# Performance work log

Measured on AMD Instinct MI355X. Metric: run time of the kernel, lower is better.

## Reference

```python
import jax, jax.numpy as jnp
import numpy as np
from jax import lax

B = 512          # scoring batch size
NC = 10          # n_classes
N_LAB = 256      # int(B * plb), plb = 0.5 (labeled indices are the first N_LAB)
TOL = 1e-3       # gtg_t
MAX_ITER = 30    # gtg_i
INTERM = 128
CH = [64, 128, 256, 512]
SZ = [32, 16, 8, 4]
EMB = 512


def setup_inputs() -> dict:
    key = jax.random.key(0)
    ks = jax.random.split(key, 16)
    inp = {}
    for i, (c, s) in enumerate(zip(CH, SZ)):
        inp["feat%d" % i] = jax.random.normal(ks[i], (B, c, s, s), jnp.float32)
        inp["conv_w%d" % i] = jax.random.normal(ks[4 + i], (c, c, 3, 3), jnp.float32) * 0.05
        inp["conv_b%d" % i] = jnp.zeros((c,), jnp.float32)
        inp["bn_g%d" % i] = jnp.ones((c,), jnp.float32)
        inp["bn_b%d" % i] = jnp.zeros((c,), jnp.float32)
        inp["lin_w%d" % i] = jax.random.normal(ks[8 + i], (INTERM, c), jnp.float32) * 0.05
        inp["lin_b%d" % i] = jnp.zeros((INTERM,), jnp.float32)
    inp["fin_w"] = jax.random.normal(ks[12], (1, 4 * INTERM), jnp.float32) * 0.05
    inp["fin_b"] = jnp.zeros((1,), jnp.float32)
    inp["embedds"] = jax.random.normal(ks[13], (B, EMB), jnp.float32)
    inp["labels"] = jax.random.randint(ks[14], (B,), 0, NC)
    return inp


def _branch(x, cw, cb, g, b, lw, lb):
    # Conv3x3(same) -> BatchNorm (train mode, batch stats, eps=1e-5) -> ReLU -> GAP -> Linear -> ReLU
    y = lax.conv_general_dilated(x, cw, (1, 1), 'SAME',
                                 dimension_numbers=('NCHW', 'OIHW', 'NCHW')) + cb[None, :, None, None]
    m = y.mean(axis=(0, 2, 3), keepdims=True)
    v = ((y - m) ** 2).mean(axis=(0, 2, 3), keepdims=True)  # biased variance (train-mode BN)
    y = jax.nn.relu(g[None, :, None, None] * (y - m) * lax.rsqrt(v + 1e-5) + b[None, :, None, None])
    y = y.mean(axis=(2, 3))  # AvgPool2d(feature_size) == global average pool -> [B, C]
    return jax.nn.relu(y @ lw.T + lb)


def _gtg(E, labels):
    # get_A_e_d: pairwise euclidean distances clamped to [0.1, 1.0]
    sq = jnp.sum(E * E, axis=1)
    d2 = jnp.maximum(sq[:, None] + sq[None, :] - 2.0 * (E @ E.T), 0.0)
    A0 = jnp.clip(jnp.sqrt(d2), 0.1, 1.0)
    # rbf kernel: 7th nearest neighbor (ascending for 'e_d') gives per-sample sigma
    seventh = E[jnp.argsort(A0, axis=1)[:, 6]]
    sig = jnp.clip(jnp.sqrt(jnp.sum((E - seventh) ** 2, axis=1)), 0.1, 1.0)
    A = jnp.clip(jnp.exp(-(A0 ** 2) / (sig[:, None] * sig[None, :])), 0.0, 1.0)
    # threshold strategy 'mean' with AM_function == 'e_d': A = where(A > mean(A), 1, A)
    A = jnp.where(A > A.mean(), 1.0, A)
    # AM_strategy 'mixed' with 'e_d': flip only the labeled x labeled block
    A = A.at[:N_LAB, :N_LAB].set(1.0 - A[:N_LAB, :N_LAB])
    # get_X: one-hot for labeled (first N_LAB), uniform 1/NC for unlabeled
    X0 = jnp.concatenate([jax.nn.one_hot(labels[:N_LAB], NC, dtype=jnp.float32),
                          jnp.full((B - N_LAB, NC), 1.0 / NC, jnp.float32)], axis=0)
    hist0 = jnp.zeros((B, MAX_ITER), jnp.float32)

    def cond(c):
        return (c[3] > TOL) & (c[2] < MAX_ITER)

    def body(c):
        X, h, i, _ = c
        Xn = X * (A @ X)
        Xn = Xn / jnp.sum(Xn, axis=1, keepdims=True)
        ent = -jnp.sum(jnp.where(Xn > 0, Xn * jnp.log(Xn), 0.0), axis=1)
        h = lax.dynamic_update_slice(h, ent[:, None], (0, i))
        return (Xn, h, i + 1, jnp.linalg.norm(Xn - X))

    X, h, _, _ = lax.while_loop(cond, body, (X0, hist0, jnp.int32(0), jnp.float32(jnp.inf)))
    return h.mean(axis=1), X  # ent_strategy == 'mean'


def reference(feat0, feat1, feat2, feat3,
              conv_w0, conv_b0, bn_g0, bn_b0, lin_w0, lin_b0,
              conv_w1, conv_b1, bn_g1, bn_b1, lin_w1, lin_b1,
              conv_w2, conv_b2, bn_g2, bn_b2, lin_w2, lin_b2,
              conv_w3, conv_b3, bn_g3, bn_b3, lin_w3, lin_b3,
              fin_w, fin_b, embedds, labels):
    o0 = _branch(feat0, conv_w0, conv_b0, bn_g0, bn_b0, lin_w0, lin_b0)
    o1 = _branch(feat1, conv_w1, conv_b1, bn_g1, bn_b1, lin_w1, lin_b1)
    o2 = _branch(feat2, conv_w2, conv_b2, bn_g2, bn_b2, lin_w2, lin_b2)
    o3 = _branch(feat3, conv_w3, conv_b3, bn_g3, bn_b3, lin_w3, lin_b3)
    y_pred = (jnp.concatenate([o0, o1, o2, o3], axis=1) @ fin_w.T + fin_b)[:, 0]
    y_true, X = _gtg(embedds, labels)
    labeled_mask = jnp.arange(B) < N_LAB
    return (y_pred, y_true, X, labeled_mask)
```

## Files before the change

### kernel.cpp

```cpp
#include <hip/hip_runtime.h>
#include <hip/hip_bf16.h>
#include <math.h>

static constexpr int kNC = 10;
static constexpr int kNLab = 256;
static constexpr int kMaxIter = 30;

using short8 = __attribute__((ext_vector_type(8))) short;
using f32x4  = __attribute__((ext_vector_type(4))) float;

__device__ __forceinline__ unsigned short f2bf(float f) {
  unsigned int u = __float_as_uint(f);
  u += 0x7FFFu + ((u >> 16) & 1u);
  return (unsigned short)(u >> 16);
}
__device__ __forceinline__ float bf2f(unsigned short u) {
  return __uint_as_float(((unsigned int)u) << 16);
}

template <int C, int S>
__global__ __launch_bounds__(256) void xpack_kernel(const float* __restrict__ x,
                                                    unsigned short* __restrict__ xp) {
  __shared__ float t[C][S + 1];
  const int n = blockIdx.x / S, h = blockIdx.x % S;
  const float* src = x + (size_t)n * C * S * S;
  for (int e = threadIdx.x; e < C * S; e += 256) {
    int c = e / S, w = e % S;
    t[c][w] = src[((size_t)c * S + h) * S + w];
  }
  __syncthreads();
  unsigned short* dst = xp + ((size_t)(n * S + h) * S) * C;
  for (int e = threadIdx.x; e < C * S; e += 256) {
    int w = e / C, c = e % C;
    dst[(size_t)w * C + c] = f2bf(t[c][w]);
  }
}

__global__ void wpack_all(const float* __restrict__ w0, const float* __restrict__ w1,
                          const float* __restrict__ w2, const float* __restrict__ w3,
                          unsigned short* __restrict__ wpk) {
  int idx = blockIdx.x * 256 + threadIdx.x;
  if (idx >= 3133440) return;
  const float* w; int C, off;
  if (idx < 36864)        { w = w0; C = 64;  off = 0; }
  else if (idx < 184320)  { w = w1; C = 128; off = 36864; }
  else if (idx < 774144)  { w = w2; C = 256; off = 184320; }
  else                    { w = w3; C = 512; off = 774144; }
  int e = idx - off;
  int CO16T = C / 16, CIK = C / 32;
  int e8 = e & 7, l = (e >> 3) & 63;
  int rest = e >> 9;
  int co16 = rest % CO16T;
  int rest2 = rest / CO16T;
  int cik = rest2 % CIK, tap = rest2 / CIK;
  int co = co16 * 16 + (l & 15);
  int ci = cik * 32 + (l >> 4) * 8 + e8;
  wpk[idx] = f2bf(w[((size_t)co * C + ci) * 9 + tap]);
}

template <int C, int S, int NI, int NR, int WV, int BF, int MODE>
__global__ __launch_bounds__(WV * 64)
void conv_mfma(const unsigned short* __restrict__ xp, const unsigned short* __restrict__ wpk,
               const float* __restrict__ bias, unsigned short* __restrict__ y,
               float* __restrict__ psum, float* __restrict__ psq, int npart, int partBase,
               const float* __restrict__ scale, const float* __restrict__ shift,
               float* __restrict__ pp, int pxGlobalBase) {
  constexpr int SS = S * S;
  constexpr int PXB = NI * NR * S;
  constexpr int TPB = WV * 64;
  constexpr int HR = NR + 2, HC = S + 2;
  constexpr int CIK = C / 32, CO16T = C / 16;
  constexpr int UNITS = NI * HR * HC * 4;
  constexpr int NU = (UNITS + TPB - 1) / TPB;
  static_assert(WV * BF * 16 == PXB, "wave px mismatch");
  static_assert(MODE != 2 || BF == 4, "MODE2 assumes 64px/wave");
  __shared__ __align__(16) char xs[NI * HR * HC * 80];

  const int tid = threadIdx.x;
  const int wv = tid >> 6, l = tid & 63, l15 = l & 15, l4 = l >> 4;
  const int coblk = blockIdx.y;
  const int co_base = coblk * 64;
  const int pxb = blockIdx.x * PXB;
  const int n_t = pxb / SS;
  const int r0 = (pxb % SS) / S;

  int pxoff[BF];
#pragma unroll
  for (int bf = 0; bf < BF; ++bf) {
    int pxloc = wv * (BF * 16) + bf * 16 + l15;
    int ii = pxloc / (NR * S);
    int rr = (pxloc % (NR * S)) / S;
    int cc = pxloc % S;
    pxoff[bf] = ((ii * HR + rr) * HC + cc) * 80 + l4 * 16;
  }

  f32x4 acc[4][BF];
#pragma unroll
  for (int a = 0; a < 4; ++a)
#pragma unroll
    for (int b = 0; b < BF; ++b) acc[a][b] = (f32x4){0.f, 0.f, 0.f, 0.f};

  uint4 vreg[NU];
  auto loadU = [&](int cik) {
#pragma unroll
    for (int k = 0; k < NU; ++k) {
      int u = tid + k * TPB;
      uint4 v = {0u, 0u, 0u, 0u};
      if (u < UNITS) {
        int k16 = u & 3;
        int t = u >> 2;
        int hc = t % HC;
        int t2 = t / HC;
        int hr = t2 % HR;
        int ii = t2 / HR;
        int row = r0 + hr - 1, col = hc - 1;
        if (row >= 0 && row < S && col >= 0 && col < S)
          v = *(const uint4*)(xp + ((size_t)((n_t + ii) * S + row) * S + col) * C + cik * 32 + k16 * 8);
      }
      vreg[k] = v;
    }
  };

  loadU(0);
  for (int cik = 0; cik < CIK; ++cik) {
    __syncthreads();
#pragma unroll
    for (int k = 0; k < NU; ++k) {
      int u = tid + k * TPB;
      if (u < UNITS) *(uint4*)(xs + (u >> 2) * 80 + (u & 3) * 16) = vreg[k];
    }
    __syncthreads();
    if (cik + 1 < CIK) loadU(cik + 1);
#pragma unroll
    for (int tap = 0; tap < 9; ++tap) {
      const int tapoff = ((tap / 3) * HC + (tap % 3)) * 80;
      short8 wf[4], xf[BF];
#pragma unroll
      for (int af = 0; af < 4; ++af)
        wf[af] = *(const short8*)(wpk + ((size_t)((tap * CIK + cik) * CO16T + coblk * 4 + af) * 64 + l) * 8);
#pragma unroll
      for (int bf = 0; bf < BF; ++bf)
        xf[bf] = *(const short8*)(xs + pxoff[bf] + tapoff);
#pragma unroll
      for (int af = 0; af < 4; ++af)
#pragma unroll
        for (int bf = 0; bf < BF; ++bf)
          acc[af][bf] = __builtin_amdgcn_mfma_f32_16x16x32_bf16(wf[af], xf[bf], acc[af][bf], 0, 0, 0);
    }
  }

#pragma unroll
  for (int af = 0; af < 4; ++af) {
    const int co0 = co_base + af * 16 + l4 * 4;
    float4 bv = *(const float4*)(bias + co0);
    float s[4] = {0.f, 0.f, 0.f, 0.f}, q[4] = {0.f, 0.f, 0.f, 0.f};
    float4 sc4, sh4;
    if (MODE == 2) {
      sc4 = *(const float4*)(scale + co0);
      sh4 = *(const float4*)(shift + co0);
    }
#pragma unroll
    for (int bf = 0; bf < BF; ++bf) {
      float o[4];
#pragma unroll
      for (int r = 0; r < 4; ++r) o[r] = acc[af][bf][r] + ((const float*)&bv)[r];
      if (MODE == 0) {
        ushort4 pk;
        pk.x = f2bf(o[0]); pk.y = f2bf(o[1]); pk.z = f2bf(o[2]); pk.w = f2bf(o[3]);
        size_t px = (size_t)(pxb + wv * (BF * 16) + bf * 16 + l15);
        *(ushort4*)(y + px * C + co0) = pk;
      }
      if (MODE == 2) {
#pragma unroll
        for (int r = 0; r < 4; ++r)
          s[r] += fmaxf(fmaf(((const float*)&sc4)[r], o[r], ((const float*)&sh4)[r]), 0.f);
      } else {
#pragma unroll
        for (int r = 0; r < 4; ++r) { s[r] += o[r]; q[r] += o[r] * o[r]; }
      }
    }
#pragma unroll
    for (int m = 1; m < 16; m <<= 1) {
#pragma unroll
      for (int r = 0; r < 4; ++r) {
        s[r] += __shfl_xor(s[r], m);
        if (MODE != 2) q[r] += __shfl_xor(q[r], m);
      }
    }
    if (l15 == 0) {
      if (MODE == 2) {
        int n = (pxGlobalBase + pxb) / SS;
        int qw = ((pxGlobalBase + pxb) % SS) / 64 + wv;
#pragma unroll
        for (int r = 0; r < 4; ++r)
          pp[((size_t)(n * C + co0 + r)) * 16 + qw] = s[r];
      } else {
        int part = partBase + blockIdx.x * WV + wv;
#pragma unroll
        for (int r = 0; r < 4; ++r) {
          psum[(size_t)(co0 + r) * npart + part] = s[r];
          psq[(size_t)(co0 + r) * npart + part] = q[r];
        }
      }
    }
  }
}

__global__ __launch_bounds__(256)
void stats2_kernel(const float* __restrict__ psum, const float* __restrict__ psq,
                   const float* __restrict__ g, const float* __restrict__ bb,
                   float* __restrict__ scale, float* __restrict__ shift,
                   int npart, float invN) {
  int c = blockIdx.x;
  __shared__ float rs[256], rq[256];
  float s = 0.f, q = 0.f;
  for (int p = threadIdx.x; p < npart; p += 256) {
    s += psum[(size_t)c * npart + p];
    q += psq[(size_t)c * npart + p];
  }
  rs[threadIdx.x] = s; rq[threadIdx.x] = q;
  __syncthreads();
  for (int st = 128; st; st >>= 1) {
    if (threadIdx.x < st) { rs[threadIdx.x] += rs[threadIdx.x + st]; rq[threadIdx.x] += rq[threadIdx.x + st]; }
    __syncthreads();
  }
  if (threadIdx.x == 0) {
    float m = rs[0] * invN;
    float v = rq[0] * invN - m * m;
    float sc = g[c] / sqrtf(v + 1e-5f);
    scale[c] = sc;
    shift[c] = bb[c] - m * sc;
  }
}

template <int C, int S>
__global__ __launch_bounds__(256)
void pool_lin(const unsigned short* __restrict__ y, const float* __restrict__ scale,
              const float* __restrict__ shift, const float* __restrict__ lw,
              const float* __restrict__ lb, float* __restrict__ oc, int brOff) {
  constexpr int SS = S * S;
  int n = blockIdx.x;
  const unsigned short* yr = y + (size_t)n * SS * C;
  __shared__ float pl[C];
  if (C >= 256) {
    for (int co = threadIdx.x; co < C; co += 256) {
      float sc = scale[co], sh = shift[co], s = 0.f;
      for (int p = 0; p < SS; ++p) s += fmaxf(fmaf(sc, bf2f(yr[(size_t)p * C + co]), sh), 0.f);
      pl[co] = s * (1.f / SS);
    }
  } else {
    constexpr int G = 256 / C;
    int co = threadIdx.x % C;
    int sl = threadIdx.x / C;
    float sc = scale[co], sh = shift[co], s = 0.f;
    for (int p = sl; p < SS; p += G) s += fmaxf(fmaf(sc, bf2f(yr[(size_t)p * C + co]), sh), 0.f);
    __shared__ float red[256];
    red[threadIdx.x] = s;
    __syncthreads();
    if (threadIdx.x < C) {
      float t = 0.f;
      for (int gg = 0; gg < G; ++gg) t += red[gg * C + co];
      pl[co] = t * (1.f / SS);
    }
  }
  __syncthreads();
  if (threadIdx.x < 128) {
    int j = threadIdx.x;
    const float* wr = lw + (size_t)j * C;
    float s = 0.f;
    for (int t = 0; t < C; ++t) s = fmaf(pl[t], wr[t], s);
    s += lb[j];
    oc[n * 512 + brOff + j] = fmaxf(s, 0.f);
  }
}

__global__ void poolfin_kernel(const float* __restrict__ pp, float* __restrict__ pooled) {
  int i = blockIdx.x * 256 + threadIdx.x;
  if (i >= 512 * 64) return;
  float s = 0.f;
  for (int qn = 0; qn < 16; ++qn) s += pp[(size_t)i * 16 + qn];
  pooled[i] = s * (1.f / 1024.f);
}

__global__ void lin_kernel(const float* __restrict__ pooled, const float* __restrict__ lw,
                           const float* __restrict__ lb, float* __restrict__ oc,
                           int C, int brOff) {
  int idx = blockIdx.x * 256 + threadIdx.x;
  if (idx >= 512 * 128) return;
  int j = idx & 127, n = idx >> 7;
  const float4* pr = (const float4*)(pooled + (size_t)n * C);
  const float4* wr = (const float4*)(lw + (size_t)j * C);
  float s = 0.f;
  for (int t = 0; t < C / 4; ++t) {
    float4 a = pr[t], b = wr[t];
    s += a.x * b.x + a.y * b.y + a.z * b.z + a.w * b.w;
  }
  s += lb[j];
  oc[n * 512 + brOff + j] = fmaxf(s, 0.f);
}

__global__ void ypred_kernel(const float* __restrict__ oc, const float* __restrict__ fw,
                             const float* __restrict__ fb, float* __restrict__ out) {
  int wv = threadIdx.x >> 6, l = threadIdx.x & 63;
  int n = blockIdx.x * 4 + wv;
  float s = 0.f;
  for (int k = l; k < 512; k += 64) s += oc[n * 512 + k] * fw[k];
#pragma unroll
  for (int m = 32; m; m >>= 1) s += __shfl_down(s, m);
  if (l == 0) out[n] = s + fb[0];
}

__global__ void sqnorm_kernel(const float* __restrict__ E, float* __restrict__ sq) {
  int wv = threadIdx.x >> 6, l = threadIdx.x & 63;
  int n = blockIdx.x * 4 + wv;
  const float* row = E + (size_t)n * 512;
  float s = 0.f;
  for (int k = l; k < 512; k += 64) { float v = row[k]; s += v * v; }
#pragma unroll
  for (int m = 32; m; m >>= 1) s += __shfl_down(s, m);
  if (l == 0) sq[n] = s;
}

__global__ __launch_bounds__(256) void a0_kernel(const float* __restrict__ E,
                                                 const float* __restrict__ sq,
                                                 float* __restrict__ A0) {
  int bi = blockIdx.x / 32, bj = blockIdx.x % 32;
  int ti = threadIdx.x % 16, tj = threadIdx.x / 16;
  __shared__ float Ei[16][68], Ej[16][68];
  float acc = 0.f;
  for (int k0 = 0; k0 < 512; k0 += 64) {
    for (int e = threadIdx.x; e < 1024; e += 256) {
      int rr = e >> 6, cc = e & 63;
      Ei[rr][cc] = E[(size_t)(bi * 16 + rr) * 512 + k0 + cc];
      Ej[rr][cc] = E[(size_t)(bj * 16 + rr) * 512 + k0 + cc];
    }
    __syncthreads();
#pragma unroll 16
    for (int kk = 0; kk < 64; ++kk) acc = fmaf(Ei[tj][kk], Ej[ti][kk], acc);
    __syncthreads();
  }
  int i = bi * 16 + tj, j = bj * 16 + ti;
  float d2 = fmaxf(sq[i] + sq[j] - 2.f * acc, 0.f);
  A0[(size_t)i * 512 + j] = fminf(fmaxf(sqrtf(d2), 0.1f), 1.0f);
}

__global__ void seventh_kernel(const float* __restrict__ A0, int* __restrict__ idx7) {
  int i = blockIdx.x * 256 + threadIdx.x;
  if (i >= 512) return;
  float v[7]; int ix[7];
#pragma unroll
  for (int t = 0; t < 7; ++t) { v[t] = 3.4e38f; ix[t] = 0; }
  const float* row = A0 + (size_t)i * 512;
  for (int j = 0; j < 512; ++j) {
    float a = row[j];
    if (a < v[6]) {
      int pos = 6;
      while (pos > 0 && a < v[pos - 1]) { v[pos] = v[pos - 1]; ix[pos] = ix[pos - 1]; --pos; }
      v[pos] = a; ix[pos] = j;
    }
  }
  idx7[i] = ix[6];
}

__global__ void sig_kernel(const float* __restrict__ E, const int* __restrict__ idx7,
                           float* __restrict__ sig) {
  int wv = threadIdx.x >> 6, l = threadIdx.x & 63;
  int n = blockIdx.x * 4 + wv;
  const float* r1 = E + (size_t)n * 512;
  const float* r2 = E + (size_t)idx7[n] * 512;
  float s = 0.f;
  for (int k = l; k < 512; k += 64) { float d = r1[k] - r2[k]; s += d * d; }
#pragma unroll
  for (int m = 32; m; m >>= 1) s += __shfl_down(s, m);
  if (l == 0) sig[n] = fminf(fmaxf(sqrtf(s), 0.1f), 1.0f);
}

__global__ void aexp_kernel(const float* __restrict__ A0, const float* __restrict__ sig,
                            float* __restrict__ A, float* __restrict__ part) {
  int t = blockIdx.x * 256 + threadIdx.x;
  int base = t * 4;
  int i = base >> 9, j0 = base & 511;
  float si = sig[i];
  float4 a = *(const float4*)(A0 + base);
  float4 o;
  o.x = fminf(fmaxf(expf(-a.x * a.x / (si * sig[j0 + 0])), 0.f), 1.f);
  o.y = fminf(fmaxf(expf(-a.y * a.y / (si * sig[j0 + 1])), 0.f), 1.f);
  o.z = fminf(fmaxf(expf(-a.z * a.z / (si * sig[j0 + 2])), 0.f), 1.f);
  o.w = fminf(fmaxf(expf(-a.w * a.w / (si * sig[j0 + 3])), 0.f), 1.f);
  *(float4*)(A + base) = o;
  float lsum = o.x + o.y + o.z + o.w;
#pragma unroll
  for (int m = 32; m; m >>= 1) lsum += __shfl_down(lsum, m);
  __shared__ float sred[4];
  if ((threadIdx.x & 63) == 0) sred[threadIdx.x >> 6] = lsum;
  __syncthreads();
  if (threadIdx.x == 0) part[blockIdx.x] = sred[0] + sred[1] + sred[2] + sred[3];
}

__global__ void meanred_kernel(const float* __restrict__ part, float* __restrict__ meanA) {
  if (threadIdx.x == 0 && blockIdx.x == 0) {
    float s = 0.f;
    for (int p = 0; p < 256; ++p) s += part[p];
    meanA[0] = s * (1.0f / 262144.0f);
  }
}

__global__ void thresh_kernel(float* __restrict__ A, const float* __restrict__ meanA) {
  int t = blockIdx.x * 256 + threadIdx.x;
  int base = t * 4;
  int i = base >> 9, j0 = base & 511;
  float m = meanA[0];
  float4 v = *(const float4*)(A + base);
  v.x = v.x > m ? 1.f : v.x;
  v.y = v.y > m ? 1.f : v.y;
  v.z = v.z > m ? 1.f : v.z;
  v.w = v.w > m ? 1.f : v.w;
  if (i < kNLab && j0 < kNLab) {
    v.x = 1.f - v.x; v.y = 1.f - v.y; v.z = 1.f - v.z; v.w = 1.f - v.w;
  }
  *(float4*)(A + base) = v;
}

__global__ __launch_bounds__(256)
void gtg_iters16(const float* __restrict__ A, const int* __restrict__ labels,
                 float* __restrict__ Xg, float* __restrict__ diffPart,
                 float* __restrict__ out, int* __restrict__ flags) {
  constexpr int NB = 16, RPB = 32;
  const int b = blockIdx.x, tid = threadIdx.x;
  const int pg = tid & 31, rg = tid >> 5;
  __shared__ float Xs[512][kNC];
  __shared__ float dred[8];

  float a[4][16];
  {
    const int gr0 = b * RPB + rg * 4;
#pragma unroll
    for (int rr = 0; rr < 4; ++rr) {
      const float* Ar = A + (size_t)(gr0 + rr) * 512 + pg;
#pragma unroll
      for (int jj = 0; jj < 16; ++jj) a[rr][jj] = Ar[32 * jj];
    }
  }
  for (int e = tid; e < 512 * kNC; e += 256) {
    int r = e / kNC, c = e % kNC;
    Xs[r][c] = (r < kNLab) ? ((labels[r] == c) ? 1.f : 0.f) : 0.1f;
  }
  __syncthreads();

  float entsum[4] = {0.f, 0.f, 0.f, 0.f};
  int ph = 0;
  for (int it = 0; it < kMaxIter; ++it) {
    if (it > 0) {
      float s = 0.f;
      for (int q = 0; q < NB; ++q) s += diffPart[(it - 1) * NB + q];
      if (sqrtf(s) <= 0.001f) break;
    }
    float ax[4][kNC];
#pragma unroll
    for (int rr = 0; rr < 4; ++rr)
#pragma unroll
      for (int c = 0; c < kNC; ++c) ax[rr][c] = 0.f;
#pragma unroll
    for (int jj = 0; jj < 16; ++jj) {
      int j = pg + 32 * jj;
      float xv[kNC];
#pragma unroll
      for (int c = 0; c < kNC; ++c) xv[c] = Xs[j][c];
#pragma unroll
      for (int rr = 0; rr < 4; ++rr) {
        float av = a[rr][jj];
#pragma unroll
        for (int c = 0; c < kNC; ++c) ax[rr][c] = fmaf(av, xv[c], ax[rr][c]);
      }
    }
#pragma unroll
    for (int m = 1; m < 32; m <<= 1)
#pragma unroll
      for (int rr = 0; rr < 4; ++rr)
#pragma unroll
        for (int c = 0; c < kNC; ++c) ax[rr][c] += __shfl_xor(ax[rr][c], m);
    if (pg == 0) {
      const int gr0 = b * RPB + rg * 4;
      float dpsum = 0.f;
#pragma unroll
      for (int rr = 0; rr < 4; ++rr) {
        int gi = gr0 + rr;
        float xn[kNC], ssum = 0.f;
#pragma unroll
        for (int c = 0; c < kNC; ++c) { xn[c] = Xs[gi][c] * ax[rr][c]; ssum += xn[c]; }
        float ent = 0.f;
#pragma unroll
        for (int c = 0; c < kNC; ++c) {
          float xv = xn[c] / ssum;
          if (xv > 0.f) ent -= xv * logf(xv);
          float d = xv - Xs[gi][c];
          dpsum += d * d;
          Xg[gi * kNC + c] = xv;
        }
        entsum[rr] += ent;
      }
      dred[rg] = dpsum;
    }
    __syncthreads();
    if (tid == 0) {
      float s2 = 0.f;
#pragma unroll
      for (int q = 0; q < 8; ++q) s2 += dred[q];
      diffPart[it * NB + b] = s2;
    }
    __syncthreads();
    __threadfence();
    if (tid == 0)
      __hip_atomic_store(&flags[b], ph + 1, __ATOMIC_RELEASE, __HIP_MEMORY_SCOPE_AGENT);
    if (tid < NB) {
      while (__hip_atomic_load(&flags[tid], __ATOMIC_ACQUIRE, __HIP_MEMORY_SCOPE_AGENT) <= ph)
        __builtin_amdgcn_s_sleep(1);
    }
    ++ph;
    __syncthreads();
    for (int e = tid; e < 512 * kNC; e += 256) Xs[e / kNC][e % kNC] = Xg[e];
    __syncthreads();
  }

  if (pg == 0) {
    const int gr0 = b * RPB + rg * 4;
#pragma unroll
    for (int rr = 0; rr < 4; ++rr) {
      int gi = gr0 + rr;
      out[512 + gi] = entsum[rr] * (1.0f / 30.0f);
      out[6144 + gi] = (gi < kNLab) ? 1.0f : 0.0f;
    }
  }
  for (int e = tid; e < RPB * kNC; e += 256) {
    int gi = b * RPB + e / kNC;
    out[1024 + gi * kNC + e % kNC] = Xs[gi][e % kNC];
  }
}

extern "C" void kernel_launch(void* const* d_in, const int* in_sizes, int n_in,
                              void* d_out, int out_size, void* d_ws, size_t ws_size,
                              hipStream_t stream) {
  (void)in_sizes; (void)n_in; (void)out_size;

  const float* feat[4]; const float* cw[4]; const float* cbp[4];
  const float* bg[4]; const float* bbp[4]; const float* lw[4]; const float* lbp[4];
  for (int b = 0; b < 4; ++b) {
    int base = b * 7;
    feat[b] = (const float*)d_in[base + 0];
    cw[b]  = (const float*)d_in[base + 1];
    cbp[b] = (const float*)d_in[base + 2];
    bg[b]  = (const float*)d_in[base + 3];
    bbp[b] = (const float*)d_in[base + 4];
    lw[b]  = (const float*)d_in[base + 5];
    lbp[b] = (const float*)d_in[base + 6];
  }
  const float* finw = (const float*)d_in[28];
  const float* finb = (const float*)d_in[29];
  const float* emb  = (const float*)d_in[30];
  const int* labels = (const int*)d_in[31];
  float* out = (float*)d_out;

  float* wsf = (float*)d_ws;
  unsigned short* xpad = (unsigned short*)wsf;
  unsigned short* yP   = (unsigned short*)(wsf + 4194304);
  unsigned short* wpk  = (unsigned short*)(wsf + 12582912);
  size_t off = 14149632;
  float* psum = wsf + off; off += 524288;
  float* psq  = wsf + off; off += 524288;
  float* pp   = wsf + off; off += 524288;
  float* scale = wsf + off; off += 512;
  float* shift = wsf + off; off += 512;
  float* pooled = wsf + off; off += 491520;
  float* oc = wsf + off; off += 262144;
  float* sq = wsf + off; off += 512;
  float* A0 = wsf + off; off += 262144;
  float* Am = wsf + off; off += 262144;
  float* sig = wsf + off; off += 512;
  int* idx7 = (int*)(wsf + off); off += 512;
  float* meanPart = wsf + off; off += 256;
  float* meanA = wsf + off; off += 4;
  float* Xg = wsf + off; off += 5120;
  float* diffPart = wsf + off; off += 512;
  int* flags = (int*)(wsf + off); off += 32;
  size_t yb0_off = off;
  unsigned short* yB0 = (unsigned short*)(wsf + yb0_off);
  const bool bigB0 = ws_size >= (yb0_off + 16777216) * sizeof(float);

  unsigned short* wpkB[4] = {wpk, wpk + 36864, wpk + 184320, wpk + 774144};

  wpack_all<<<(3133440 + 255) / 256, 256, 0, stream>>>(cw[0], cw[1], cw[2], cw[3], wpk);

  for (int c = 0; c < 2; ++c) {
    xpack_kernel<128, 16><<<256 * 16, 256, 0, stream>>>(feat[1] + (size_t)c * 8388608, xpad);
    conv_mfma<128, 16, 1, 8, 4, 2, 0><<<dim3(512, 2), 256, 0, stream>>>(
        xpad, wpkB[1], cbp[1], yP + (size_t)c * 8388608, psum, psq, 4096, c * 2048,
        nullptr, nullptr, nullptr, 0);
  }
  stats2_kernel<<<128, 256, 0, stream>>>(psum, psq, bg[1], bbp[1], scale, shift, 4096, 1.f / 131072.f);
  pool_lin<128, 16><<<512, 256, 0, stream>>>(yP, scale, shift, lw[1], lbp[1], oc, 128);

  xpack_kernel<256, 8><<<512 * 8, 256, 0, stream>>>(feat[2], xpad);
  conv_mfma<256, 8, 2, 8, 4, 2, 0><<<dim3(256, 4), 256, 0, stream>>>(
      xpad, wpkB[2], cbp[2], yP, psum, psq, 1024, 0, nullptr, nullptr, nullptr, 0);
  stats2_kernel<<<256, 256, 0, stream>>>(psum, psq, bg[2], bbp[2], scale, shift, 1024, 1.f / 32768.f);
  pool_lin<256, 8><<<512, 256, 0, stream>>>(yP, scale, shift, lw[2], lbp[2], oc, 256);

  xpack_kernel<512, 4><<<512 * 4, 256, 0, stream>>>(feat[3], xpad);
  conv_mfma<512, 4, 8, 4, 4, 2, 0><<<dim3(64, 8), 256, 0, stream>>>(
      xpad, wpkB[3], cbp[3], yP, psum, psq, 256, 0, nullptr, nullptr, nullptr, 0);
  stats2_kernel<<<512, 256, 0, stream>>>(psum, psq, bg[3], bbp[3], scale, shift, 256, 1.f / 8192.f);
  pool_lin<512, 4><<<512, 256, 0, stream>>>(yP, scale, shift, lw[3], lbp[3], oc, 384);

  if (bigB0) {
    for (int c = 0; c < 4; ++c) {
      xpack_kernel<64, 32><<<128 * 32, 256, 0, stream>>>(feat[0] + (size_t)c * 8388608, xpad);
      conv_mfma<64, 32, 1, 8, 4, 4, 0><<<dim3(512, 1), 256, 0, stream>>>(
          xpad, wpkB[0], cbp[0], yB0 + (size_t)c * 8388608, psum, psq, 8192, c * 2048,
          nullptr, nullptr, nullptr, 0);
    }
    stats2_kernel<<<64, 256, 0, stream>>>(psum, psq, bg[0], bbp[0], scale, shift, 8192, 1.f / 524288.f);
    pool_lin<64, 32><<<512, 256, 0, stream>>>(yB0, scale, shift, lw[0], lbp[0], oc, 0);
  } else {
    for (int c = 0; c < 4; ++c) {
      xpack_kernel<64, 32><<<128 * 32, 256, 0, stream>>>(feat[0] + (size_t)c * 8388608, xpad);
      conv_mfma<64, 32, 1, 8, 4, 4, 1><<<dim3(512, 1), 256, 0, stream>>>(
          xpad, wpkB[0], cbp[0], nullptr, psum, psq, 8192, c * 2048, nullptr, nullptr, nullptr, 0);
    }
    stats2_kernel<<<64, 256, 0, stream>>>(psum, psq, bg[0], bbp[0], scale, shift, 8192, 1.f / 524288.f);
    for (int c = 0; c < 4; ++c) {
      xpack_kernel<64, 32><<<128 * 32, 256, 0, stream>>>(feat[0] + (size_t)c * 8388608, xpad);
      conv_mfma<64, 32, 1, 8, 4, 4, 2><<<dim3(512, 1), 256, 0, stream>>>(
          xpad, wpkB[0], cbp[0], nullptr, nullptr, nullptr, 0, 0, scale, shift, pp, c * 131072);
    }
    poolfin_kernel<<<128, 256, 0, stream>>>(pp, pooled);
    lin_kernel<<<256, 256, 0, stream>>>(pooled, lw[0], lbp[0], oc, 64, 0);
  }

  ypred_kernel<<<128, 256, 0, stream>>>(oc, finw, finb, out);
  sqnorm_kernel<<<128, 256, 0, stream>>>(emb, sq);
  a0_kernel<<<1024, 256, 0, stream>>>(emb, sq, A0);
  seventh_kernel<<<2, 256, 0, stream>>>(A0, idx7);
  sig_kernel<<<128, 256, 0, stream>>>(emb, idx7, sig);
  aexp_kernel<<<256, 256, 0, stream>>>(A0, sig, Am, meanPart);
  meanred_kernel<<<1, 64, 0, stream>>>(meanPart, meanA);
  thresh_kernel<<<256, 256, 0, stream>>>(Am, meanA);

  hipMemsetAsync(flags, 0, 64, stream);
  gtg_iters16<<<16, 256, 0, stream>>>(Am, labels, Xg, diffPart, out, flags);
}
```

Before: 1.003 ms.

## Run GTG iterations in one block and skip fixed labeled rows

Replaces the 16-block GTG iteration kernel, which synchronised through global flags and atomics on every iteration, with a single 1024-thread block that uses only __syncthreads. It relies on the labeled rows staying one-hot: their contribution A[unlabeled, labeled]·onehot is computed once up front, and only the 256 unlabeled rows are updated each iteration. Labeled outputs (zero entropy, one-hot X) are written directly. This removes the cross-block barrier latency and half the matvec work, at the cost of using only one CU and assuming a labeled row's class sum is never zero.

```diff
diff --git a/kernel.cpp b/kernel.cpp
--- a/kernel.cpp
+++ b/kernel.cpp
@@ -421,119 +421,138 @@
   *(float4*)(A + base) = v;
 }
 
-__global__ __launch_bounds__(256)
-void gtg_iters16(const float* __restrict__ A, const int* __restrict__ labels,
-                 float* __restrict__ Xg, float* __restrict__ diffPart,
-                 float* __restrict__ out, int* __restrict__ flags) {
-  constexpr int NB = 16, RPB = 32;
-  const int b = blockIdx.x, tid = threadIdx.x;
-  const int pg = tid & 31, rg = tid >> 5;
-  __shared__ float Xs[512][kNC];
-  __shared__ float dred[8];
-
-  float a[4][16];
+__global__ __launch_bounds__(1024)
+void gtg1(const float* __restrict__ A, const int* __restrict__ labels,
+          float* __restrict__ out) {
+  const int tid = threadIdx.x;
+  const int w = tid >> 6, l = tid & 63;
+  const int rc = w & 3, g = w >> 2;
+  const int i = rc * 64 + l;
+  __shared__ float Xs[256][12];
+  __shared__ float Ls[256][12];
+  __shared__ float axred[4][256][12];
+  __shared__ float dredw[4];
+  __shared__ int labs[256];
+
+  if (tid < 256) labs[tid] = labels[tid];
+  for (int e = tid; e < 256 * 12; e += 1024)
+    (&Xs[0][0])[e] = ((e % 12) < 10) ? 0.1f : 0.f;
+  __syncthreads();
+
+  const float* Ar = A + (size_t)(256 + i) * 512;
+  float areg[64];
+#pragma unroll
+  for (int q = 0; q < 16; ++q) {
+    float4 v = *(const float4*)(Ar + 256 + g * 64 + q * 4);
+    areg[q * 4 + 0] = v.x; areg[q * 4 + 1] = v.y;
+    areg[q * 4 + 2] = v.z; areg[q * 4 + 3] = v.w;
+  }
   {
-    const int gr0 = b * RPB + rg * 4;
-#pragma unroll
-    for (int rr = 0; rr < 4; ++rr) {
-      const float* Ar = A + (size_t)(gr0 + rr) * 512 + pg;
-#pragma unroll
-      for (int jj = 0; jj < 16; ++jj) a[rr][jj] = Ar[32 * jj];
-    }
-  }
-  for (int e = tid; e < 512 * kNC; e += 256) {
-    int r = e / kNC, c = e % kNC;
-    Xs[r][c] = (r < kNLab) ? ((labels[r] == c) ? 1.f : 0.f) : 0.1f;
+    float lp[10];
+#pragma unroll
+    for (int c = 0; c < 10; ++c) lp[c] = 0.f;
+    for (int q = 0; q < 16; ++q) {
+      float4 v = *(const float4*)(Ar + g * 64 + q * 4);
+      float av[4] = {v.x, v.y, v.z, v.w};
+#pragma unroll
+      for (int k = 0; k < 4; ++k) {
+        int lab = labs[g * 64 + q * 4 + k];
+#pragma unroll
+        for (int c = 0; c < 10; ++c) lp[c] += (lab == c) ? av[k] : 0.f;
+      }
+    }
+    *(float4*)&axred[g][i][0] = make_float4(lp[0], lp[1], lp[2], lp[3]);
+    *(float4*)&axred[g][i][4] = make_float4(lp[4], lp[5], lp[6], lp[7]);
+    *(float2*)&axred[g][i][8] = make_float2(lp[8], lp[9]);
   }
   __syncthreads();
-
-  float entsum[4] = {0.f, 0.f, 0.f, 0.f};
-  int ph = 0;
+  if (g == 0) {
+    float s[10];
+#pragma unroll
+    for (int c = 0; c < 10; ++c) s[c] = 0.f;
+#pragma unroll
+    for (int q = 0; q < 4; ++q) {
+      float4 a0 = *(const float4*)&axred[q][i][0];
+      float4 a1 = *(const float4*)&axred[q][i][4];
+      float2 a2 = *(const float2*)&axred[q][i][8];
+      s[0] += a0.x; s[1] += a0.y; s[2] += a0.z; s[3] += a0.w;
+      s[4] += a1.x; s[5] += a1.y; s[6] += a1.z; s[7] += a1.w;
+      s[8] += a2.x; s[9] += a2.y;
+    }
+    *(float4*)&Ls[i][0] = make_float4(s[0], s[1], s[2], s[3]);
+    *(float4*)&Ls[i][4] = make_float4(s[4], s[5], s[6], s[7]);
+    *(float2*)&Ls[i][8] = make_float2(s[8], s[9]);
+  }
+  __syncthreads();
+
+  float entsum = 0.f;
+  float nrm2 = 1e30f;
   for (int it = 0; it < kMaxIter; ++it) {
-    if (it > 0) {
-      float s = 0.f;
-      for (int q = 0; q < NB; ++q) s += diffPart[(it - 1) * NB + q];
-      if (sqrtf(s) <= 0.001f) break;
-    }
-    float ax[4][kNC];
-#pragma unroll
-    for (int rr = 0; rr < 4; ++rr)
-#pragma unroll
-      for (int c = 0; c < kNC; ++c) ax[rr][c] = 0.f;
-#pragma unroll
-    for (int jj = 0; jj < 16; ++jj) {
-      int j = pg + 32 * jj;
-      float xv[kNC];
-#pragma unroll
-      for (int c = 0; c < kNC; ++c) xv[c] = Xs[j][c];
-#pragma unroll
-      for (int rr = 0; rr < 4; ++rr) {
-        float av = a[rr][jj];
-#pragma unroll
-        for (int c = 0; c < kNC; ++c) ax[rr][c] = fmaf(av, xv[c], ax[rr][c]);
-      }
-    }
-#pragma unroll
-    for (int m = 1; m < 32; m <<= 1)
-#pragma unroll
-      for (int rr = 0; rr < 4; ++rr)
-#pragma unroll
-        for (int c = 0; c < kNC; ++c) ax[rr][c] += __shfl_xor(ax[rr][c], m);
-    if (pg == 0) {
-      const int gr0 = b * RPB + rg * 4;
-      float dpsum = 0.f;
-#pragma unroll
-      for (int rr = 0; rr < 4; ++rr) {
-        int gi = gr0 + rr;
-        float xn[kNC], ssum = 0.f;
-#pragma unroll
-        for (int c = 0; c < kNC; ++c) { xn[c] = Xs[gi][c] * ax[rr][c]; ssum += xn[c]; }
-        float ent = 0.f;
-#pragma unroll
-        for (int c = 0; c < kNC; ++c) {
-          float xv = xn[c] / ssum;
-          if (xv > 0.f) ent -= xv * logf(xv);
-          float d = xv - Xs[gi][c];
-          dpsum += d * d;
-          Xg[gi * kNC + c] = xv;
-        }
-        entsum[rr] += ent;
-      }
-      dred[rg] = dpsum;
-    }
-    __syncthreads();
-    if (tid == 0) {
-      float s2 = 0.f;
-#pragma unroll
-      for (int q = 0; q < 8; ++q) s2 += dred[q];
-      diffPart[it * NB + b] = s2;
-    }
-    __syncthreads();
-    __threadfence();
-    if (tid == 0)
-      __hip_atomic_store(&flags[b], ph + 1, __ATOMIC_RELEASE, __HIP_MEMORY_SCOPE_AGENT);
-    if (tid < NB) {
-      while (__hip_atomic_load(&flags[tid], __ATOMIC_ACQUIRE, __HIP_MEMORY_SCOPE_AGENT) <= ph)
-        __builtin_amdgcn_s_sleep(1);
-    }
-    ++ph;
-    __syncthreads();
-    for (int e = tid; e < 512 * kNC; e += 256) Xs[e / kNC][e % kNC] = Xg[e];
-    __syncthreads();
-  }
-
-  if (pg == 0) {
-    const int gr0 = b * RPB + rg * 4;
-#pragma unroll
-    for (int rr = 0; rr < 4; ++rr) {
-      int gi = gr0 + rr;
-      out[512 + gi] = entsum[rr] * (1.0f / 30.0f);
-      out[6144 + gi] = (gi < kNLab) ? 1.0f : 0.0f;
-    }
-  }
-  for (int e = tid; e < RPB * kNC; e += 256) {
-    int gi = b * RPB + e / kNC;
-    out[1024 + gi * kNC + e % kNC] = Xs[gi][e % kNC];
+    if (it > 0 && sqrtf(nrm2) <= 0.001f) break;
+    float ax[10];
+#pragma unroll
+    for (int c = 0; c < 10; ++c) ax[c] = 0.f;
+#pragma unroll
+    for (int jj = 0; jj < 64; ++jj) {
+      const int j = g * 64 + jj;
+      float4 x0 = *(const float4*)&Xs[j][0];
+      float4 x1 = *(const float4*)&Xs[j][4];
+      float2 x2 = *(const float2*)&Xs[j][8];
+      float a = areg[jj];
+      ax[0] = fmaf(a, x0.x, ax[0]); ax[1] = fmaf(a, x0.y, ax[1]);
+      ax[2] = fmaf(a, x0.z, ax[2]); ax[3] = fmaf(a, x0.w, ax[3]);
+      ax[4] = fmaf(a, x1.x, ax[4]); ax[5] = fmaf(a, x1.y, ax[5]);
+      ax[6] = fmaf(a, x1.z, ax[6]); ax[7] = fmaf(a, x1.w, ax[7]);
+      ax[8] = fmaf(a, x2.x, ax[8]); ax[9] = fmaf(a, x2.y, ax[9]);
+    }
+    *(float4*)&axred[g][i][0] = make_float4(ax[0], ax[1], ax[2], ax[3]);
+    *(float4*)&axred[g][i][4] = make_float4(ax[4], ax[5], ax[6], ax[7]);
+    *(float2*)&axred[g][i][8] = make_float2(ax[8], ax[9]);
+    __syncthreads();
+    if (g == 0) {
+      float s[10];
+#pragma unroll
+      for (int c = 0; c < 10; ++c) s[c] = Ls[i][c];
+#pragma unroll
+      for (int q = 0; q < 4; ++q) {
+        float4 a0 = *(const float4*)&axred[q][i][0];
+        float4 a1 = *(const float4*)&axred[q][i][4];
+        float2 a2 = *(const float2*)&axred[q][i][8];
+        s[0] += a0.x; s[1] += a0.y; s[2] += a0.z; s[3] += a0.w;
+        s[4] += a1.x; s[5] += a1.y; s[6] += a1.z; s[7] += a1.w;
+        s[8] += a2.x; s[9] += a2.y;
+      }
+      float xn[10], ssum = 0.f;
+#pragma unroll
+      for (int c = 0; c < 10; ++c) { xn[c] = Xs[i][c] * s[c]; ssum += xn[c]; }
+      float ent = 0.f, dp = 0.f;
+#pragma unroll
+      for (int c = 0; c < 10; ++c) {
+        float xv = xn[c] / ssum;
+        if (xv > 0.f) ent -= xv * logf(xv);
+        float d = xv - Xs[i][c];
+        dp += d * d;
+        Xs[i][c] = xv;
+      }
+      entsum += ent;
+#pragma unroll
+      for (int m = 1; m < 64; m <<= 1) dp += __shfl_xor(dp, m);
+      if (l == 0) dredw[rc] = dp;
+    }
+    __syncthreads();
+    nrm2 = dredw[0] + dredw[1] + dredw[2] + dredw[3];
+  }
+
+  if (g == 0) out[512 + 256 + i] = entsum * (1.0f / 30.0f);
+  for (int e = tid; e < 256; e += 1024) {
+    out[512 + e] = 0.f;
+    out[6144 + e] = 1.f;
+    out[6144 + 256 + e] = 0.f;
+  }
+  for (int e = tid; e < 2560; e += 1024) {
+    int r = e / 10, c = e % 10;
+    out[1024 + e] = (labs[r] == c) ? 1.f : 0.f;
+    out[1024 + 2560 + e] = Xs[r][c];
   }
 }
 
@@ -579,9 +598,6 @@
   int* idx7 = (int*)(wsf + off); off += 512;
   float* meanPart = wsf + off; off += 256;
   float* meanA = wsf + off; off += 4;
-  float* Xg = wsf + off; off += 5120;
-  float* diffPart = wsf + off; off += 512;
-  int* flags = (int*)(wsf + off); off += 32;
   size_t yb0_off = off;
   unsigned short* yB0 = (unsigned short*)(wsf + yb0_off);
   const bool bigB0 = ws_size >= (yb0_off + 16777216) * sizeof(float);
@@ -645,6 +661,5 @@
   meanred_kernel<<<1, 64, 0, stream>>>(meanPart, meanA);
   thresh_kernel<<<256, 256, 0, stream>>>(Am, meanA);
 
-  hipMemsetAsync(flags, 0, 64, stream);
-  gtg_iters16<<<16, 256, 0, stream>>>(Am, labels, Xg, diffPart, out, flags);
-}
+  gtg1<<<1, 1024, 0, stream>>>(Am, labels, out);
+}
```

Result: no change. 1.008 ms (+0.5%).
